# Kernel optimization log

Measured on AMD Instinct MI355X. Metric: run time of the kernel, lower is better.

Reference implementation:

```python
import jax, jax.numpy as jnp
import numpy as np

B, N, D, S, H = 64, 4096, 256, 8, 512
ITERS = 3
EPS = 1e-8
SCALE = D ** -0.5
LN_EPS = 1e-5


def _ln(x, w, b):
    mu = jnp.mean(x, axis=-1, keepdims=True)
    var = jnp.var(x, axis=-1, keepdims=True)
    return (x - mu) * jax.lax.rsqrt(var + LN_EPS) * w + b


def setup_inputs() -> dict:
    key = jax.random.key(0)
    ks = jax.random.split(key, 20)
    g = lambda k, shape, s=0.02: jax.random.normal(k, shape, dtype=jnp.float32) * s
    return {
        "inputs": jax.random.normal(ks[0], (B, N, D), dtype=jnp.float32),
        "query_pos": jax.random.uniform(ks[1], (1, S, D), dtype=jnp.float32),
        "wq": g(ks[2], (D, D)), "bq": jnp.zeros((D,), jnp.float32),
        "wk": g(ks[3], (D, D)), "bk": jnp.zeros((D,), jnp.float32),
        "wv": g(ks[4], (D, D)), "bv": jnp.zeros((D,), jnp.float32),
        "w_ih": g(ks[5], (3 * D, D)), "b_ih": jnp.zeros((3 * D,), jnp.float32),
        "w_hh": g(ks[6], (3 * D, D)), "b_hh": jnp.zeros((3 * D,), jnp.float32),
        "w1": g(ks[7], (H, D)), "b1": jnp.zeros((H,), jnp.float32),
        "w2": g(ks[8], (D, H)), "b2": jnp.zeros((D,), jnp.float32),
        "ln_in_w": jnp.ones((D,), jnp.float32), "ln_in_b": jnp.zeros((D,), jnp.float32),
        "ln_s_w": jnp.ones((D,), jnp.float32), "ln_s_b": jnp.zeros((D,), jnp.float32),
        "ln_ff_w": jnp.ones((D,), jnp.float32), "ln_ff_b": jnp.zeros((D,), jnp.float32),
    }


def _step(slots, k, v, wq, bq, w_ih, b_ih, w_hh, b_hh, w1, b1, w2, b2,
          ln_s_w, ln_s_b, ln_ff_w, ln_ff_b):
    s = _ln(slots, ln_s_w, ln_s_b)
    q = s @ wq.T + bq                                  # [B,S,D]
    dots = jnp.einsum('bid,bjd->bij', q, k) * SCALE    # [B,S,N]
    attn = jax.nn.softmax(dots, axis=1) + EPS          # softmax over slots
    attn = attn / jnp.sum(attn, axis=-1, keepdims=True)
    updates = jnp.einsum('bjd,bij->bid', v, attn)      # [B,S,D]
    # GRUCell(input=updates, hidden=slots), PyTorch gate order r,z,n
    gx = updates @ w_ih.T + b_ih
    gh = slots @ w_hh.T + b_hh
    xr, xz, xn = jnp.split(gx, 3, axis=-1)
    hr, hz, hn = jnp.split(gh, 3, axis=-1)
    r = jax.nn.sigmoid(xr + hr)
    z = jax.nn.sigmoid(xz + hz)
    n = jnp.tanh(xn + r * hn)
    h = (1.0 - z) * n + z * slots
    ff = jnp.maximum(_ln(h, ln_ff_w, ln_ff_b) @ w1.T + b1, 0.0) @ w2.T + b2
    return h + ff


def reference(inputs, query_pos, wq, bq, wk, bk, wv, bv,
              w_ih, b_ih, w_hh, b_hh, w1, b1, w2, b2,
              ln_in_w, ln_in_b, ln_s_w, ln_s_b, ln_ff_w, ln_ff_b):
    b = inputs.shape[0]
    slots = jnp.broadcast_to(query_pos, (b, S, D))
    x = _ln(inputs, ln_in_w, ln_in_b)
    k = x @ wk.T + bk
    v = x @ wv.T + bv
    step = lambda s: _step(s, k, v, wq, bq, w_ih, b_ih, w_hh, b_hh,
                           w1, b1, w2, b2, ln_s_w, ln_s_b, ln_ff_w, ln_ff_b)
    for _ in range(ITERS):
        slots = step(slots)
    slots = step(jax.lax.stop_gradient(slots))
    return slots
```

## Files before the change

### kernel.cpp

```cpp
#include <hip/hip_runtime.h>
#include <hip/hip_bf16.h>

#define DEV __device__ __forceinline__
typedef unsigned short u16;
using s16x8  = __attribute__((ext_vector_type(8))) short;
using f32x4v = __attribute__((ext_vector_type(4))) float;

constexpr float SCALE  = 0.0625f;
constexpr float EPS    = 1e-8f;
constexpr float LN_EPS = 1e-5f;

DEV u16 f2bf(float f) {
    __hip_bfloat16 h = __float2bfloat16(f);
    u16 u; __builtin_memcpy(&u, &h, 2); return u;
}
DEV float bf2f(u16 u) {
    unsigned int x = ((unsigned int)u) << 16;
    float f; __builtin_memcpy(&f, &x, 4); return f;
}
DEV float ld1(const void* p, size_t i, int bf) {
    return bf ? bf2f(((const u16*)p)[i]) : ((const float*)p)[i];
}
DEV s16x8 pack8(float4 a, float4 b) {
    s16x8 o;
    o[0]=(short)f2bf(a.x); o[1]=(short)f2bf(a.y); o[2]=(short)f2bf(a.z); o[3]=(short)f2bf(a.w);
    o[4]=(short)f2bf(b.x); o[5]=(short)f2bf(b.y); o[6]=(short)f2bf(b.z); o[7]=(short)f2bf(b.w);
    return o;
}
DEV float warp_sum64(float v) {
    v += __shfl_xor(v, 1);  v += __shfl_xor(v, 2);  v += __shfl_xor(v, 4);
    v += __shfl_xor(v, 8);  v += __shfl_xor(v, 16); v += __shfl_xor(v, 32);
    return v;
}
DEV float sigf(float x) { return 1.f / (1.f + expf(-x)); }

__global__ void k_sniff(const void* __restrict__ x, int* __restrict__ flag) {
    int lane = threadIdx.x;
    u16 u = ((const u16*)x)[lane * 2];
    float v = bf2f(u);
    bool bad = !(fabsf(v) <= 1024.0f);
    unsigned long long m = __ballot(bad);
    if (lane == 0) *flag = (m == 0ull) ? 1 : 0;
}

__global__ __launch_bounds__(256) void k_prep_misc(
    const void* bq, const void* bk, const void* bv, const void* bih, const void* bhh,
    const void* b1, const void* b2, const void* liw, const void* lib,
    const void* lsw, const void* lsb, const void* lfw, const void* lfb,
    float* o_bq, float* o_bk, float* o_bv, float* o_bih, float* o_bhh,
    float* o_b1, float* o_b2, float* o_liw, float* o_lib,
    float* o_lsw, float* o_lsb, float* o_lfw, float* o_lfb,
    const int* flagp) {
    int bf = *flagp;
    int i = blockIdx.x * 256 + threadIdx.x;
    if (i < 256) { o_bq[i]  = ld1(bq,  i, bf); return; } i -= 256;
    if (i < 256) { o_bk[i]  = ld1(bk,  i, bf); return; } i -= 256;
    if (i < 256) { o_bv[i]  = ld1(bv,  i, bf); return; } i -= 256;
    if (i < 768) { o_bih[i] = ld1(bih, i, bf); return; } i -= 768;
    if (i < 768) { o_bhh[i] = ld1(bhh, i, bf); return; } i -= 768;
    if (i < 512) { o_b1[i]  = ld1(b1,  i, bf); return; } i -= 512;
    if (i < 256) { o_b2[i]  = ld1(b2,  i, bf); return; } i -= 256;
    if (i < 256) { o_liw[i] = ld1(liw, i, bf); return; } i -= 256;
    if (i < 256) { o_lib[i] = ld1(lib, i, bf); return; } i -= 256;
    if (i < 256) { o_lsw[i] = ld1(lsw, i, bf); return; } i -= 256;
    if (i < 256) { o_lsb[i] = ld1(lsb, i, bf); return; } i -= 256;
    if (i < 256) { o_lfw[i] = ld1(lfw, i, bf); return; } i -= 256;
    if (i < 256) { o_lfb[i] = ld1(lfb, i, bf); }
}

__global__ __launch_bounds__(256) void k_prep_w(
    const void* wq, const void* wv, const void* wk,
    const void* wih, const void* whh, const void* w1, const void* w2,
    u16* wqT_b, u16* wvT_b, u16* wk2_b, u16* wih_b, u16* whh_b, u16* w1_b, u16* w2_b,
    const float* __restrict__ liw, const int* flagp) {
    int bf = *flagp;
    int i = blockIdx.x * 256 + threadIdx.x;
    if (i < 65536)  { int c=i>>8, d=i&255; wqT_b[i] = f2bf(ld1(wq, (size_t)d*256+c, bf)); return; } i -= 65536;
    if (i < 65536)  { int c=i>>8, d=i&255; wvT_b[i] = f2bf(ld1(wv, (size_t)d*256+c, bf)); return; } i -= 65536;
    if (i < 65536)  { int n=i>>8, d=i&255; wk2_b[i] = f2bf(ld1(wk, (size_t)d*256+n, bf) * liw[n]); return; } i -= 65536;
    if (i < 196608) { wih_b[i] = f2bf(ld1(wih, i, bf)); return; } i -= 196608;
    if (i < 196608) { whh_b[i] = f2bf(ld1(whh, i, bf)); return; } i -= 196608;
    if (i < 131072) { w1_b[i]  = f2bf(ld1(w1,  i, bf)); return; } i -= 131072;
    if (i < 131072) { w2_b[i]  = f2bf(ld1(w2,  i, bf)); }
}

__global__ __launch_bounds__(256) void k_prep_m(const void* __restrict__ wk,
    const float* __restrict__ liw, const float* __restrict__ lib,
    const float* __restrict__ bk_f, float* __restrict__ m1p, float* __restrict__ m2p,
    const int* flagp) {
    int bf = *flagp;
    int wave = threadIdx.x >> 6, lane = threadIdx.x & 63;
    int d = blockIdx.x * 4 + wave;
    float s1 = 0.f, s2 = 0.f;
#pragma unroll
    for (int t = 0; t < 4; t++) {
        int c = lane * 4 + t;
        float w = ld1(wk, (size_t)d * 256 + c, bf);
        s1 += w * lib[c];
        s2 += w * liw[c];
    }
    s1 = warp_sum64(s1); s2 = warp_sum64(s2);
    if (lane == 0) { m1p[d] = s1 + bk_f[d]; m2p[d] = -s2; }
}

__global__ __launch_bounds__(256) void k_prep_u(
    const void* __restrict__ wq, const void* __restrict__ wk, const void* __restrict__ wih,
    const float* __restrict__ m1p, const float* __restrict__ m2p,
    const float* __restrict__ bq_f, const float* __restrict__ bv_f,
    const float* __restrict__ liw,
    float* __restrict__ u1, float* __restrict__ u2, float* __restrict__ bq2,
    float* __restrict__ wibv, float* __restrict__ c12, const int* flagp) {
    int bf = *flagp;
    int wave = threadIdx.x >> 6, lane = threadIdx.x & 63;
    int idx = blockIdx.x * 4 + wave;
    if (idx >= 1538) return;
    float s = 0.f;
#pragma unroll
    for (int t = 0; t < 4; t++) {
        int d = lane * 4 + t;
        if (idx < 256)       s += ld1(wq, (size_t)d*256 + idx, bf) * m1p[d];
        else if (idx < 512)  s += ld1(wq, (size_t)d*256 + (idx-256), bf) * m2p[d];
        else if (idx < 768)  s += bq_f[d] * ld1(wk, (size_t)d*256 + (idx-512), bf);
        else if (idx < 1536) s += ld1(wih, (size_t)(idx-768)*256 + d, bf) * bv_f[d];
        else if (idx == 1536) s += bq_f[d] * m1p[d];
        else                  s += bq_f[d] * m2p[d];
    }
    s = warp_sum64(s);
    if (lane == 0) {
        if (idx < 256)       u1[idx] = s;
        else if (idx < 512)  u2[idx-256] = s;
        else if (idx < 768)  bq2[idx-512] = s * liw[idx-512];
        else if (idx < 1536) wibv[idx-768] = s;
        else                 c12[idx-1536] = s;
    }
}

__global__ __launch_bounds__(256) void k_stats(const void* __restrict__ x,
                                               float* __restrict__ mu,
                                               float* __restrict__ rs,
                                               const int* flagp) {
    int bf = *flagp;
    int wave = threadIdx.x >> 6, lane = threadIdx.x & 63;
    int row  = blockIdx.x * 4 + wave;
    float v[4];
    if (bf) {
        u16 a4[4];
        __builtin_memcpy(a4, (const u16*)x + (size_t)row * 256 + lane * 4, 8);
#pragma unroll
        for (int i = 0; i < 4; i++) v[i] = bf2f(a4[i]);
    } else {
        float4 f = *(const float4*)((const float*)x + (size_t)row * 256 + lane * 4);
        v[0]=f.x; v[1]=f.y; v[2]=f.z; v[3]=f.w;
    }
    float s  = v[0]+v[1]+v[2]+v[3];
    float s2 = v[0]*v[0]+v[1]*v[1]+v[2]*v[2]+v[3]*v[3];
    s = warp_sum64(s); s2 = warp_sum64(s2);
    if (lane == 0) {
        float m = s * (1.f/256.f);
        mu[row] = m;
        rs[row] = rsqrtf(s2 * (1.f/256.f) - m*m + LN_EPS);
    }
}

__global__ __launch_bounds__(256) void k_prep_s(const void* __restrict__ qp,
    const float* __restrict__ lsw, const float* __restrict__ lsb,
    const float* __restrict__ u1, const float* __restrict__ u2, const float* __restrict__ c12,
    float* __restrict__ slots, u16* __restrict__ Acat, u16* __restrict__ s_b,
    float* __restrict__ kap, float* __restrict__ lam, const int* flagp) {
    int bf = *flagp;
    int m = blockIdx.x;
    int s_ = m & 7, d = threadIdx.x;
    float v = ld1(qp, (size_t)s_ * 256 + d, bf);
    slots[(size_t)m*256 + d]   = v;
    Acat[(size_t)m*512 + 256 + d] = f2bf(v);
    __shared__ float red[16];
    float su = warp_sum64(v), sq = warp_sum64(v*v);
    int wave = threadIdx.x >> 6, lane = threadIdx.x & 63;
    if (lane == 0) { red[wave] = su; red[4+wave] = sq; }
    __syncthreads();
    float S1 = red[0]+red[1]+red[2]+red[3], S2 = red[4]+red[5]+red[6]+red[7];
    float muv = S1*(1.f/256.f);
    float rsv = rsqrtf(S2*(1.f/256.f) - muv*muv + LN_EPS);
    float sn = (v - muv)*rsv*lsw[d] + lsb[d];
    s_b[(size_t)m*256 + d] = f2bf(sn);
    float ks = warp_sum64(sn * u1[d]), ls = warp_sum64(sn * u2[d]);
    if (lane == 0) { red[8+wave] = ks; red[12+wave] = ls; }
    __syncthreads();
    if (threadIdx.x == 0) {
        kap[m] = red[8]+red[9]+red[10]+red[11] + c12[0];
        lam[m] = red[12]+red[13]+red[14]+red[15] + c12[1];
    }
}

template<bool OUT_BF16, bool RELU>
__global__ __launch_bounds__(256) void gemm64(
    const u16* __restrict__ A, const u16* __restrict__ W,
    const float* __restrict__ bias, void* __restrict__ outp, int Nn, int K) {
    int m0 = blockIdx.x * 64, n0 = blockIdx.y * 64;
    int tid = threadIdx.x;
    int wave = tid >> 6, lane = tid & 63, quad = lane >> 4, l15 = lane & 15;
    int wm = wave >> 1, wn = wave & 1;
    __shared__ __attribute__((aligned(16))) u16 A_s[64*40];
    __shared__ __attribute__((aligned(16))) u16 B_s[64*40];
    f32x4v acc[2][2];
#pragma unroll
    for (int i = 0; i < 2; i++)
#pragma unroll
        for (int j = 0; j < 2; j++) acc[i][j] = (f32x4v){0.f,0.f,0.f,0.f};
    int r0 = tid >> 2, seg = tid & 3;
    int nkc = K >> 5;
    for (int kc = 0; kc < nkc; ++kc) {
        s16x8 a0 = *(const s16x8*)(A + (size_t)(m0 + r0)*K + kc*32 + seg*8);
        s16x8 b0 = *(const s16x8*)(W + (size_t)(n0 + r0)*K + kc*32 + seg*8);
        __syncthreads();
        *(s16x8*)(A_s + r0*40 + seg*8) = a0;
        *(s16x8*)(B_s + r0*40 + seg*8) = b0;
        __syncthreads();
        s16x8 af[2], bfr[2];
#pragma unroll
        for (int t = 0; t < 2; t++) af[t]  = *(const s16x8*)(A_s + (wm*32 + t*16 + l15)*40 + quad*8);
#pragma unroll
        for (int t = 0; t < 2; t++) bfr[t] = *(const s16x8*)(B_s + (wn*32 + t*16 + l15)*40 + quad*8);
#pragma unroll
        for (int ti = 0; ti < 2; ti++)
#pragma unroll
            for (int tj = 0; tj < 2; tj++)
                acc[ti][tj] = __builtin_amdgcn_mfma_f32_16x16x32_bf16(af[ti], bfr[tj], acc[ti][tj], 0, 0, 0);
    }
#pragma unroll
    for (int tj = 0; tj < 2; tj++) {
        int colg = n0 + wn*32 + tj*16 + l15;
        float bv_ = bias ? bias[colg] : 0.f;
#pragma unroll
        for (int ti = 0; ti < 2; ti++) {
            int rowb = m0 + wm*32 + ti*16 + quad*4;
#pragma unroll
            for (int r = 0; r < 4; r++) {
                float v = acc[ti][tj][r] + bv_;
                if (RELU) v = fmaxf(v, 0.f);
                if (OUT_BF16) ((u16*)outp)[(size_t)(rowb + r)*Nn + colg] = f2bf(v);
                else          ((float*)outp)[(size_t)(rowb + r)*Nn + colg] = v;
            }
        }
    }
}

__global__ __launch_bounds__(256) void k_big(const u16* __restrict__ Wc2_b,
    const u16* __restrict__ whh_b, const float* __restrict__ bih_f,
    const float* __restrict__ bhh_f, const float* __restrict__ wibv,
    u16* __restrict__ Wbig, float* __restrict__ bbig) {
    int idx = blockIdx.x * 256 + threadIdx.x;
    int n = idx >> 9, k = idx & 511;
    u16 v;
    if (n < 512)      v = (k < 256) ? Wc2_b[(size_t)n*256 + k] : whh_b[(size_t)n*256 + (k-256)];
    else if (n < 768) v = (k < 256) ? Wc2_b[(size_t)n*256 + k] : (u16)0;
    else              v = (k < 256) ? (u16)0 : whh_b[(size_t)(n-256)*256 + (k-256)];
    Wbig[idx] = v;
    if (idx < 1024) {
        float bb;
        if (idx < 512)      bb = bih_f[idx] + wibv[idx] + bhh_f[idx];
        else if (idx < 768) bb = bih_f[idx] + wibv[idx];
        else                bb = bhh_f[idx-256];
        bbig[idx] = bb;
    }
}

__global__ __launch_bounds__(256) void k_attn(
    const void* __restrict__ xraw, const u16* __restrict__ q2b,
    const float* __restrict__ kap, const float* __restrict__ lam,
    const float* __restrict__ mu, const float* __restrict__ rs,
    const int* __restrict__ flagp,
    float* __restrict__ Zp, float* __restrict__ Rp, float* __restrict__ Tp) {
    int bf = *flagp;
    int jcc = blockIdx.x;
    int b   = blockIdx.y;
    int tid = threadIdx.x;
    int wave = tid >> 6, lane = tid & 63, quad = lane >> 4, l15 = lane & 15;
    __shared__ __attribute__((aligned(16))) u16 q_s[16*264];
    __shared__ __attribute__((aligned(16))) u16 a_s[16*72];
    __shared__ __attribute__((aligned(16))) u16 T_s[32*520];
    __shared__ float kl_s[32];
    {
        int row = tid >> 5, seg = tid & 31;
        s16x8 qv = *(const s16x8*)(q2b + (size_t)(b*8 + row)*256 + seg*8);
        *(s16x8*)(q_s + row*264 + seg*8) = qv;
        s16x8 z = {0,0,0,0,0,0,0,0};
        *(s16x8*)(q_s + (8+row)*264 + seg*8) = z;
    }
    if (tid < 16) {
        kl_s[tid]      = (tid < 8) ? kap[b*8 + tid] : 0.f;
        kl_s[16 + tid] = (tid < 8) ? lam[b*8 + tid] : 0.f;
    }
    f32x4v accz[4];
#pragma unroll
    for (int t = 0; t < 4; t++) accz[t] = (f32x4v){0.f,0.f,0.f,0.f};
    float rtot[4] = {0.f,0.f,0.f,0.f}, ttot[4] = {0.f,0.f,0.f,0.f};

    for (int sub = 0; sub < 2; ++sub) {
        size_t jbase = (size_t)b*4096 + (size_t)(jcc*2 + sub)*64;
        __syncthreads();
#pragma unroll
        for (int it = 0; it < 8; ++it) {
            int j = it*8 + (tid >> 5);
            int cb = tid & 31;
            s16x8 val;
            if (bf) {
                val = *(const s16x8*)((const u16*)xraw + (jbase + j)*256 + cb*8);
            } else {
                const float4* sf = (const float4*)((const float*)xraw + (jbase + j)*256 + cb*8);
                float4 f0 = sf[0], f1 = sf[1];
                val = pack8(f0, f1);
            }
            *(s16x8*)(T_s + cb*520 + j*8) = val;
        }
        __syncthreads();
        f32x4v accd = (f32x4v){0.f,0.f,0.f,0.f};
        int jb16 = wave * 16;
#pragma unroll
        for (int kc = 0; kc < 8; ++kc) {
            s16x8 af = *(const s16x8*)(q_s + l15*264 + kc*32 + quad*8);
            s16x8 bv = *(const s16x8*)(T_s + (kc*4 + quad)*520 + (jb16 + l15)*8);
            accd = __builtin_amdgcn_mfma_f32_16x16x32_bf16(af, bv, accd, 0, 0, 0);
        }
        int jg = (int)jbase + jb16 + l15;
        float rsj = rs[jg], mrj = mu[jg] * rsj;
        float dv[4];
#pragma unroll
        for (int r = 0; r < 4; r++)
            dv[r] = SCALE*(rsj*accd[r] + mrj*kl_s[16 + quad*4 + r] + kl_s[quad*4 + r]);
        float mx = fmaxf(fmaxf(dv[0], dv[1]), fmaxf(dv[2], dv[3]));
        mx = fmaxf(mx, __shfl_xor(mx, 16));
        float ev[4];
        float sum = 0.f;
#pragma unroll
        for (int r = 0; r < 4; r++) { ev[r] = expf(dv[r] - mx); sum += ev[r]; }
        sum += __shfl_xor(sum, 16);
        float inv = 1.f / sum;
#pragma unroll
        for (int r = 0; r < 4; r++) {
            float a = ev[r]*inv + EPS;
            rtot[r] += a;
            ttot[r] += a * mrj;
            a_s[(quad*4 + r)*72 + jb16 + l15] = f2bf(a * rsj);
        }
        __syncthreads();
#pragma unroll
        for (int kc2 = 0; kc2 < 2; ++kc2) {
            s16x8 af2 = *(const s16x8*)(a_s + l15*72 + kc2*32 + quad*8);
#pragma unroll
            for (int ct = 0; ct < 4; ++ct) {
                int c = wave*64 + ct*16 + l15;
                int cb = c >> 3, e = c & 7;
                s16x8 bv;
#pragma unroll
                for (int t = 0; t < 8; t++)
                    bv[t] = (short)T_s[cb*520 + (kc2*32 + quad*8 + t)*8 + e];
                accz[ct] = __builtin_amdgcn_mfma_f32_16x16x32_bf16(af2, bv, accz[ct], 0, 0, 0);
            }
        }
    }
    if (quad < 2) {
#pragma unroll
        for (int ct = 0; ct < 4; ++ct) {
            int c = wave*64 + ct*16 + l15;
#pragma unroll
            for (int r = 0; r < 4; r++)
                Zp[((size_t)(b*32 + jcc)*8 + quad*4 + r)*256 + c] = accz[ct][r];
        }
    }
#pragma unroll
    for (int r = 0; r < 4; r++) {
        rtot[r] += __shfl_xor(rtot[r], 1);
        rtot[r] += __shfl_xor(rtot[r], 2);
        rtot[r] += __shfl_xor(rtot[r], 4);
        rtot[r] += __shfl_xor(rtot[r], 8);
        ttot[r] += __shfl_xor(ttot[r], 1);
        ttot[r] += __shfl_xor(ttot[r], 2);
        ttot[r] += __shfl_xor(ttot[r], 4);
        ttot[r] += __shfl_xor(ttot[r], 8);
    }
    if (l15 == 0 && quad < 2) {
        int base = ((b*32 + jcc)*4 + wave)*8 + quad*4;
#pragma unroll
        for (int r = 0; r < 4; r++) { Rp[base + r] = rtot[r]; Tp[base + r] = ttot[r]; }
    }
}

__global__ __launch_bounds__(256) void k_reduce(const float* __restrict__ Zp,
    const float* __restrict__ Rp, const float* __restrict__ Tp,
    const float* __restrict__ liw, const float* __restrict__ lib,
    u16* __restrict__ Acat) {
    int m = blockIdx.x;
    int b = m >> 3, i = m & 7, d = threadIdx.x;
    float z = 0.f;
#pragma unroll
    for (int c = 0; c < 32; c++) z += Zp[((size_t)(b*32 + c)*8 + i)*256 + d];
    float rv = 0.f, tv = 0.f;
    if (d < 128) {
        rv = Rp[(size_t)(b*128 + d)*8 + i];
        tv = Tp[(size_t)(b*128 + d)*8 + i];
    }
    __shared__ float redR[4], redT[4];
    rv = warp_sum64(rv); tv = warp_sum64(tv);
    int wave = d >> 6, lane = d & 63;
    if (lane == 0) { redR[wave] = rv; redT[wave] = tv; }
    __syncthreads();
    float R = redR[0]+redR[1]+redR[2]+redR[3];
    float T = redT[0]+redT[1]+redT[2]+redT[3];
    float ys = (liw[d]*(z - T) + lib[d]*R) / R;
    Acat[(size_t)m*512 + d] = f2bf(ys);
}

__global__ __launch_bounds__(256) void k_gates(const float* __restrict__ g,
    const float* __restrict__ slots, const float* __restrict__ lfw,
    const float* __restrict__ lfb, float* __restrict__ h, u16* __restrict__ hln_b) {
    int m = blockIdx.x, d = threadIdx.x;
    const float* gm = g + (size_t)m*1024;
    float r = sigf(gm[d]);
    float z = sigf(gm[256 + d]);
    float nn = tanhf(gm[512 + d] + r * gm[768 + d]);
    float hv = (1.f - z)*nn + z*slots[(size_t)m*256 + d];
    h[(size_t)m*256 + d] = hv;
    __shared__ float red[8];
    float su = warp_sum64(hv), sq = warp_sum64(hv*hv);
    int wave = threadIdx.x >> 6, lane = threadIdx.x & 63;
    if (lane == 0) { red[wave] = su; red[4+wave] = sq; }
    __syncthreads();
    float S1 = red[0]+red[1]+red[2]+red[3], S2 = red[4]+red[5]+red[6]+red[7];
    float muv = S1*(1.f/256.f);
    float rsv = rsqrtf(S2*(1.f/256.f) - muv*muv + LN_EPS);
    hln_b[(size_t)m*256 + d] = f2bf((hv - muv)*rsv*lfw[d] + lfb[d]);
}

__global__ __launch_bounds__(256) void k_residual(const float* __restrict__ h,
    const float* __restrict__ ff2, const float* __restrict__ lsw,
    const float* __restrict__ lsb, const float* __restrict__ u1,
    const float* __restrict__ u2, const float* __restrict__ c12,
    float* __restrict__ slots, u16* __restrict__ Acat, u16* __restrict__ s_b,
    float* __restrict__ kap, float* __restrict__ lam) {
    int m = blockIdx.x, d = threadIdx.x;
    float sv = h[(size_t)m*256 + d] + ff2[(size_t)m*256 + d];
    slots[(size_t)m*256 + d] = sv;
    Acat[(size_t)m*512 + 256 + d] = f2bf(sv);
    __shared__ float red[16];
    float su = warp_sum64(sv), sq = warp_sum64(sv*sv);
    int wave = threadIdx.x >> 6, lane = threadIdx.x & 63;
    if (lane == 0) { red[wave] = su; red[4+wave] = sq; }
    __syncthreads();
    float S1 = red[0]+red[1]+red[2]+red[3], S2 = red[4]+red[5]+red[6]+red[7];
    float muv = S1*(1.f/256.f);
    float rsv = rsqrtf(S2*(1.f/256.f) - muv*muv + LN_EPS);
    float sn = (sv - muv)*rsv*lsw[d] + lsb[d];
    s_b[(size_t)m*256 + d] = f2bf(sn);
    float ks = warp_sum64(sn * u1[d]), ls = warp_sum64(sn * u2[d]);
    if (lane == 0) { red[8+wave] = ks; red[12+wave] = ls; }
    __syncthreads();
    if (threadIdx.x == 0) {
        kap[m] = red[8]+red[9]+red[10]+red[11] + c12[0];
        lam[m] = red[12]+red[13]+red[14]+red[15] + c12[1];
    }
}

__global__ __launch_bounds__(256) void k_out(const float* __restrict__ slots,
                                             void* __restrict__ out, const int* flagp) {
    int bf = *flagp;
    int i = blockIdx.x * 256 + threadIdx.x;
    if (bf) ((u16*)out)[i] = f2bf(slots[i]);
    else    ((float*)out)[i] = slots[i];
}

extern "C" void kernel_launch(void* const* d_in, const int* in_sizes, int n_in,
                              void* d_out, int out_size, void* d_ws, size_t ws_size,
                              hipStream_t stream) {
    (void)in_sizes; (void)n_in; (void)out_size; (void)ws_size;
    const void* inputs    = d_in[0];
    const void* query_pos = d_in[1];
    const void* wq   = d_in[2];  const void* bq   = d_in[3];
    const void* wk   = d_in[4];  const void* bk   = d_in[5];
    const void* wv   = d_in[6];  const void* bv   = d_in[7];
    const void* w_ih = d_in[8];  const void* b_ih = d_in[9];
    const void* w_hh = d_in[10]; const void* b_hh = d_in[11];
    const void* w1   = d_in[12]; const void* b1   = d_in[13];
    const void* w2   = d_in[14]; const void* b2   = d_in[15];
    const void* ln_in_w = d_in[16]; const void* ln_in_b = d_in[17];
    const void* ln_s_w  = d_in[18]; const void* ln_s_b  = d_in[19];
    const void* ln_ff_w = d_in[20]; const void* ln_ff_b = d_in[21];

    char* w = (char*)d_ws;
    size_t off = 0;
    auto alloc = [&](size_t bytes) -> void* {
        void* p = w + off;
        off = (off + bytes + 255) & ~(size_t)255;
        return p;
    };
    float* Zp     = (float*)alloc(16777216);
    float* gates  = (float*)alloc(2097152);
    u16*   Wbig_b = (u16*)alloc(1048576);
    u16*   Wc2_b  = (u16*)alloc(393216);
    u16*   Wc_b   = (u16*)alloc(131072);
    u16*   wqT_b  = (u16*)alloc(131072);
    u16*   wvT_b  = (u16*)alloc(131072);
    u16*   wk2_b  = (u16*)alloc(131072);
    u16*   wih_b  = (u16*)alloc(393216);
    u16*   whh_b  = (u16*)alloc(393216);
    u16*   w1_b   = (u16*)alloc(262144);
    u16*   w2_b   = (u16*)alloc(262144);
    float* mu     = (float*)alloc(1048576);
    float* rs     = (float*)alloc(1048576);
    float* slots  = (float*)alloc(524288);
    u16*   s_b    = (u16*)alloc(262144);
    u16*   Acat   = (u16*)alloc(524288);
    u16*   q2_b   = (u16*)alloc(262144);
    float* h      = (float*)alloc(524288);
    u16*   hln_b  = (u16*)alloc(262144);
    u16*   ff1_b  = (u16*)alloc(524288);
    float* ff2    = (float*)alloc(524288);
    float* Rp     = (float*)alloc(262144);
    float* Tp     = (float*)alloc(262144);
    float* bq_f   = (float*)alloc(1024);
    float* bk_f   = (float*)alloc(1024);
    float* bv_f   = (float*)alloc(1024);
    float* bih_f  = (float*)alloc(3072);
    float* bhh_f  = (float*)alloc(3072);
    float* b1_f   = (float*)alloc(2048);
    float* b2_f   = (float*)alloc(1024);
    float* liw_f  = (float*)alloc(1024);
    float* lib_f  = (float*)alloc(1024);
    float* lsw_f  = (float*)alloc(1024);
    float* lsb_f  = (float*)alloc(1024);
    float* lfw_f  = (float*)alloc(1024);
    float* lfb_f  = (float*)alloc(1024);
    float* m1p    = (float*)alloc(1024);
    float* m2p    = (float*)alloc(1024);
    float* u1     = (float*)alloc(1024);
    float* u2     = (float*)alloc(1024);
    float* bq2    = (float*)alloc(1024);
    float* wibv   = (float*)alloc(3072);
    float* bbig   = (float*)alloc(4096);
    float* c12    = (float*)alloc(256);
    float* kap    = (float*)alloc(2048);
    float* lam    = (float*)alloc(2048);
    int*   flag   = (int*)alloc(256);

    k_sniff<<<1, 64, 0, stream>>>(inputs, flag);
    k_prep_misc<<<18, 256, 0, stream>>>(bq, bk, bv, b_ih, b_hh, b1, b2,
                                        ln_in_w, ln_in_b, ln_s_w, ln_s_b, ln_ff_w, ln_ff_b,
                                        bq_f, bk_f, bv_f, bih_f, bhh_f, b1_f, b2_f,
                                        liw_f, lib_f, lsw_f, lsb_f, lfw_f, lfb_f, flag);
    k_stats<<<65536, 256, 0, stream>>>(inputs, mu, rs, flag);
    k_prep_w<<<3328, 256, 0, stream>>>(wq, wv, wk, w_ih, w_hh, w1, w2,
                                       wqT_b, wvT_b, wk2_b, wih_b, whh_b, w1_b, w2_b,
                                       liw_f, flag);
    k_prep_m<<<64, 256, 0, stream>>>(wk, liw_f, lib_f, bk_f, m1p, m2p, flag);
    k_prep_u<<<385, 256, 0, stream>>>(wq, wk, w_ih, m1p, m2p, bq_f, bv_f, liw_f,
                                      u1, u2, bq2, wibv, c12, flag);
    k_prep_s<<<512, 256, 0, stream>>>(query_pos, lsw_f, lsb_f, u1, u2, c12,
                                      slots, Acat, s_b, kap, lam, flag);
    gemm64<true, false><<<dim3(4, 4), 256, 0, stream>>>(wk2_b, wqT_b, nullptr, Wc_b, 256, 256);
    gemm64<true, false><<<dim3(12, 4), 256, 0, stream>>>(wih_b, wvT_b, nullptr, Wc2_b, 256, 256);
    k_big<<<2048, 256, 0, stream>>>(Wc2_b, whh_b, bih_f, bhh_f, wibv, Wbig_b, bbig);

    for (int step = 0; step < 4; ++step) {
        gemm64<true, false><<<dim3(8, 4), 256, 0, stream>>>(s_b, Wc_b, bq2, q2_b, 256, 256);
        k_attn<<<dim3(32, 64), 256, 0, stream>>>(inputs, q2_b, kap, lam, mu, rs, flag, Zp, Rp, Tp);
        k_reduce<<<512, 256, 0, stream>>>(Zp, Rp, Tp, liw_f, lib_f, Acat);
        gemm64<false, false><<<dim3(8, 16), 256, 0, stream>>>(Acat, Wbig_b, bbig, gates, 1024, 512);
        k_gates<<<512, 256, 0, stream>>>(gates, slots, lfw_f, lfb_f, h, hln_b);
        gemm64<true, true ><<<dim3(8, 8), 256, 0, stream>>>(hln_b, w1_b, b1_f, ff1_b, 512, 256);
        gemm64<false, false><<<dim3(8, 4), 256, 0, stream>>>(ff1_b, w2_b, b2_f, ff2, 256, 512);
        k_residual<<<512, 256, 0, stream>>>(h, ff2, lsw_f, lsb_f, u1, u2, c12,
                                            slots, Acat, s_b, kap, lam);
    }
    k_out<<<512, 256, 0, stream>>>(slots, d_out, flag);
}
```

Baseline: 809.6 us.

## Precompute bf16 row-major and transposed input copies once, reuse across attention steps

A new conversion kernel reads the input once, computes layernorm statistics, and writes both a bf16 row-major copy and a bf16 channel-major transposed copy. The attention kernel then loads MFMA operands directly from these copies instead of converting fp32 to bf16 and transposing through shared memory every iteration, and it drops the per-element scalar LDS gathers. This removes repeated conversion and LDS transpose work across the four steps. In exchange it adds 256 MB of workspace writes up front and keeps per-step global reads roughly as large.

```diff
diff --git a/kernel.cpp b/kernel.cpp
--- a/kernel.cpp
+++ b/kernel.cpp
@@ -20,12 +20,6 @@
 }
 DEV float ld1(const void* p, size_t i, int bf) {
     return bf ? bf2f(((const u16*)p)[i]) : ((const float*)p)[i];
-}
-DEV s16x8 pack8(float4 a, float4 b) {
-    s16x8 o;
-    o[0]=(short)f2bf(a.x); o[1]=(short)f2bf(a.y); o[2]=(short)f2bf(a.z); o[3]=(short)f2bf(a.w);
-    o[4]=(short)f2bf(b.x); o[5]=(short)f2bf(b.y); o[6]=(short)f2bf(b.z); o[7]=(short)f2bf(b.w);
-    return o;
 }
 DEV float warp_sum64(float v) {
     v += __shfl_xor(v, 1);  v += __shfl_xor(v, 2);  v += __shfl_xor(v, 4);
@@ -135,31 +129,56 @@
     }
 }
 
-__global__ __launch_bounds__(256) void k_stats(const void* __restrict__ x,
-                                               float* __restrict__ mu,
-                                               float* __restrict__ rs,
-                                               const int* flagp) {
-    int bf = *flagp;
-    int wave = threadIdx.x >> 6, lane = threadIdx.x & 63;
-    int row  = blockIdx.x * 4 + wave;
-    float v[4];
-    if (bf) {
-        u16 a4[4];
-        __builtin_memcpy(a4, (const u16*)x + (size_t)row * 256 + lane * 4, 8);
-#pragma unroll
-        for (int i = 0; i < 4; i++) v[i] = bf2f(a4[i]);
-    } else {
-        float4 f = *(const float4*)((const float*)x + (size_t)row * 256 + lane * 4);
-        v[0]=f.x; v[1]=f.y; v[2]=f.z; v[3]=f.w;
-    }
-    float s  = v[0]+v[1]+v[2]+v[3];
-    float s2 = v[0]*v[0]+v[1]*v[1]+v[2]*v[2]+v[3]*v[3];
-    s = warp_sum64(s); s2 = warp_sum64(s2);
-    if (lane == 0) {
-        float m = s * (1.f/256.f);
-        mu[row] = m;
-        rs[row] = rsqrtf(s2 * (1.f/256.f) - m*m + LN_EPS);
-    }
+__global__ __launch_bounds__(256) void k_conv(const void* __restrict__ x,
+    u16* __restrict__ XB, u16* __restrict__ XT,
+    float* __restrict__ mu, float* __restrict__ rs, const int* flagp) {
+    int bf = *flagp;
+    int jt = blockIdx.x;
+    int b  = blockIdx.y;
+    int tid = threadIdx.x;
+    int j = tid >> 2, q = tid & 3;
+    size_t rowg = (size_t)b * 4096 + jt * 64 + j;
+    __shared__ u16 LT[256 * 72];
+    float s = 0.f, s2 = 0.f;
+#pragma unroll
+    for (int cc = 0; cc < 16; ++cc) {
+        int c0 = cc * 16 + q * 4;
+        float v[4];
+        if (bf) {
+            u16 a4[4];
+            __builtin_memcpy(a4, (const u16*)x + rowg * 256 + c0, 8);
+#pragma unroll
+            for (int e = 0; e < 4; e++) v[e] = bf2f(a4[e]);
+        } else {
+            float4 f = *(const float4*)((const float*)x + rowg * 256 + c0);
+            v[0] = f.x; v[1] = f.y; v[2] = f.z; v[3] = f.w;
+        }
+        u16 b4[4];
+#pragma unroll
+        for (int e = 0; e < 4; e++) {
+            s += v[e]; s2 += v[e] * v[e];
+            b4[e] = f2bf(v[e]);
+            LT[(c0 + e) * 72 + j] = b4[e];
+        }
+        __builtin_memcpy(XB + rowg * 256 + c0, b4, 8);
+    }
+    s  += __shfl_xor(s, 1);   s  += __shfl_xor(s, 2);
+    s2 += __shfl_xor(s2, 1);  s2 += __shfl_xor(s2, 2);
+    if (q == 0) {
+        float m = s * (1.f / 256.f);
+        mu[rowg] = m;
+        rs[rowg] = rsqrtf(s2 * (1.f / 256.f) - m * m + LN_EPS);
+    }
+    __syncthreads();
+    int c = tid;
+    s16x8 seg[8];
+#pragma unroll
+    for (int k = 0; k < 8; ++k)
+        seg[k] = *(const s16x8*)(LT + c * 72 + k * 8);
+    u16* dst = XT + ((size_t)b * 256 + c) * 4096 + jt * 64;
+#pragma unroll
+    for (int k = 0; k < 8; ++k)
+        *(s16x8*)(dst + k * 8) = seg[k];
 }
 
 __global__ __launch_bounds__(256) void k_prep_s(const void* __restrict__ qp,
@@ -266,19 +285,17 @@
 }
 
 __global__ __launch_bounds__(256) void k_attn(
-    const void* __restrict__ xraw, const u16* __restrict__ q2b,
+    const u16* __restrict__ XB, const u16* __restrict__ XT,
+    const u16* __restrict__ q2b,
     const float* __restrict__ kap, const float* __restrict__ lam,
     const float* __restrict__ mu, const float* __restrict__ rs,
-    const int* __restrict__ flagp,
     float* __restrict__ Zp, float* __restrict__ Rp, float* __restrict__ Tp) {
-    int bf = *flagp;
     int jcc = blockIdx.x;
     int b   = blockIdx.y;
     int tid = threadIdx.x;
     int wave = tid >> 6, lane = tid & 63, quad = lane >> 4, l15 = lane & 15;
     __shared__ __attribute__((aligned(16))) u16 q_s[16*264];
     __shared__ __attribute__((aligned(16))) u16 a_s[16*72];
-    __shared__ __attribute__((aligned(16))) u16 T_s[32*520];
     __shared__ float kl_s[32];
     {
         int row = tid >> 5, seg = tid & 31;
@@ -291,39 +308,29 @@
         kl_s[tid]      = (tid < 8) ? kap[b*8 + tid] : 0.f;
         kl_s[16 + tid] = (tid < 8) ? lam[b*8 + tid] : 0.f;
     }
+    __syncthreads();
+
     f32x4v accz[4];
 #pragma unroll
     for (int t = 0; t < 4; t++) accz[t] = (f32x4v){0.f,0.f,0.f,0.f};
     float rtot[4] = {0.f,0.f,0.f,0.f}, ttot[4] = {0.f,0.f,0.f,0.f};
+    int jb16 = wave * 16;
+    const u16* xtb = XT + (size_t)b * 256 * 4096;
 
     for (int sub = 0; sub < 2; ++sub) {
-        size_t jbase = (size_t)b*4096 + (size_t)(jcc*2 + sub)*64;
-        __syncthreads();
-#pragma unroll
-        for (int it = 0; it < 8; ++it) {
-            int j = it*8 + (tid >> 5);
-            int cb = tid & 31;
-            s16x8 val;
-            if (bf) {
-                val = *(const s16x8*)((const u16*)xraw + (jbase + j)*256 + cb*8);
-            } else {
-                const float4* sf = (const float4*)((const float*)xraw + (jbase + j)*256 + cb*8);
-                float4 f0 = sf[0], f1 = sf[1];
-                val = pack8(f0, f1);
-            }
-            *(s16x8*)(T_s + cb*520 + j*8) = val;
-        }
-        __syncthreads();
+        int jloc = (jcc*2 + sub) * 64;
+        size_t rowg = (size_t)b*4096 + jloc + jb16 + l15;
+        const u16* xbp = XB + rowg*256 + quad*8;
+        s16x8 xv[8];
+#pragma unroll
+        for (int kc = 0; kc < 8; ++kc) xv[kc] = *(const s16x8*)(xbp + kc*32);
         f32x4v accd = (f32x4v){0.f,0.f,0.f,0.f};
-        int jb16 = wave * 16;
 #pragma unroll
         for (int kc = 0; kc < 8; ++kc) {
             s16x8 af = *(const s16x8*)(q_s + l15*264 + kc*32 + quad*8);
-            s16x8 bv = *(const s16x8*)(T_s + (kc*4 + quad)*520 + (jb16 + l15)*8);
-            accd = __builtin_amdgcn_mfma_f32_16x16x32_bf16(af, bv, accd, 0, 0, 0);
-        }
-        int jg = (int)jbase + jb16 + l15;
-        float rsj = rs[jg], mrj = mu[jg] * rsj;
+            accd = __builtin_amdgcn_mfma_f32_16x16x32_bf16(af, xv[kc], accd, 0, 0, 0);
+        }
+        float rsj = rs[rowg], mrj = mu[rowg] * rsj;
         float dv[4];
 #pragma unroll
         for (int r = 0; r < 4; r++)
@@ -336,26 +343,33 @@
         for (int r = 0; r < 4; r++) { ev[r] = expf(dv[r] - mx); sum += ev[r]; }
         sum += __shfl_xor(sum, 16);
         float inv = 1.f / sum;
+        float av[4];
 #pragma unroll
         for (int r = 0; r < 4; r++) {
             float a = ev[r]*inv + EPS;
             rtot[r] += a;
             ttot[r] += a * mrj;
-            a_s[(quad*4 + r)*72 + jb16 + l15] = f2bf(a * rsj);
+            av[r] = a * rsj;
+        }
+        s16x8 zv[8];
+#pragma unroll
+        for (int ct = 0; ct < 4; ++ct) {
+            int c = wave*64 + ct*16 + l15;
+#pragma unroll
+            for (int kc2 = 0; kc2 < 2; ++kc2)
+                zv[ct*2 + kc2] = *(const s16x8*)(xtb + (size_t)c*4096 + jloc + kc2*32 + quad*8);
         }
         __syncthreads();
 #pragma unroll
-        for (int kc2 = 0; kc2 < 2; ++kc2) {
-            s16x8 af2 = *(const s16x8*)(a_s + l15*72 + kc2*32 + quad*8);
-#pragma unroll
-            for (int ct = 0; ct < 4; ++ct) {
-                int c = wave*64 + ct*16 + l15;
-                int cb = c >> 3, e = c & 7;
-                s16x8 bv;
-#pragma unroll
-                for (int t = 0; t < 8; t++)
-                    bv[t] = (short)T_s[cb*520 + (kc2*32 + quad*8 + t)*8 + e];
-                accz[ct] = __builtin_amdgcn_mfma_f32_16x16x32_bf16(af2, bv, accz[ct], 0, 0, 0);
+        for (int r = 0; r < 4; r++)
+            a_s[(quad*4 + r)*72 + jb16 + l15] = f2bf(av[r]);
+        __syncthreads();
+#pragma unroll
+        for (int ct = 0; ct < 4; ++ct) {
+#pragma unroll
+            for (int kc2 = 0; kc2 < 2; ++kc2) {
+                s16x8 af2 = *(const s16x8*)(a_s + l15*72 + kc2*32 + quad*8);
+                accz[ct] = __builtin_amdgcn_mfma_f32_16x16x32_bf16(af2, zv[ct*2 + kc2], accz[ct], 0, 0, 0);
             }
         }
     }
@@ -493,6 +507,8 @@
         off = (off + bytes + 255) & ~(size_t)255;
         return p;
     };
+    u16*   XB     = (u16*)alloc(134217728);
+    u16*   XT     = (u16*)alloc(134217728);
     float* Zp     = (float*)alloc(16777216);
     float* gates  = (float*)alloc(2097152);
     u16*   Wbig_b = (u16*)alloc(1048576);
@@ -547,7 +563,7 @@
                                         ln_in_w, ln_in_b, ln_s_w, ln_s_b, ln_ff_w, ln_ff_b,
                                         bq_f, bk_f, bv_f, bih_f, bhh_f, b1_f, b2_f,
                                         liw_f, lib_f, lsw_f, lsb_f, lfw_f, lfb_f, flag);
-    k_stats<<<65536, 256, 0, stream>>>(inputs, mu, rs, flag);
+    k_conv<<<dim3(64, 64), 256, 0, stream>>>(inputs, XB, XT, mu, rs, flag);
     k_prep_w<<<3328, 256, 0, stream>>>(wq, wv, wk, w_ih, w_hh, w1, w2,
                                        wqT_b, wvT_b, wk2_b, wih_b, whh_b, w1_b, w2_b,
                                        liw_f, flag);
@@ -562,7 +578,7 @@
 
     for (int step = 0; step < 4; ++step) {
         gemm64<true, false><<<dim3(8, 4), 256, 0, stream>>>(s_b, Wc_b, bq2, q2_b, 256, 256);
-        k_attn<<<dim3(32, 64), 256, 0, stream>>>(inputs, q2_b, kap, lam, mu, rs, flag, Zp, Rp, Tp);
+        k_attn<<<dim3(32, 64), 256, 0, stream>>>(XB, XT, q2_b, kap, lam, mu, rs, Zp, Rp, Tp);
         k_reduce<<<512, 256, 0, stream>>>(Zp, Rp, Tp, liw_f, lib_f, Acat);
         gemm64<false, false><<<dim3(8, 16), 256, 0, stream>>>(Acat, Wbig_b, bbig, gates, 1024, 512);
         k_gates<<<512, 256, 0, stream>>>(gates, slots, lfw_f, lfb_f, h, hln_b);
```

Measured after the change: 899.4 us. 1.11x slower.

## Cache bf16 copy of inputs once and read it in attention steps

Applied to the files above, without the earlier changes.

The stats pass now writes a bf16 copy of the fp32 inputs to a 128 MB workspace, so each of the four attention steps reads half the bytes and skips the per-step fp32-to-bf16 conversion. The attention kernel also loads the dot-product B operand straight from global memory into registers, issues global loads before the barrier, pads the shared tile layout to cut LDS bank conflicts, and shrinks the query tile by zero-filling the unused MFMA rows in registers. The cost is one extra 128 MB write up front plus a larger workspace.

```diff
diff --git a/kernel.cpp b/kernel.cpp
--- a/kernel.cpp
+++ b/kernel.cpp
@@ -21,18 +21,14 @@
 DEV float ld1(const void* p, size_t i, int bf) {
     return bf ? bf2f(((const u16*)p)[i]) : ((const float*)p)[i];
 }
-DEV s16x8 pack8(float4 a, float4 b) {
-    s16x8 o;
-    o[0]=(short)f2bf(a.x); o[1]=(short)f2bf(a.y); o[2]=(short)f2bf(a.z); o[3]=(short)f2bf(a.w);
-    o[4]=(short)f2bf(b.x); o[5]=(short)f2bf(b.y); o[6]=(short)f2bf(b.z); o[7]=(short)f2bf(b.w);
-    return o;
-}
 DEV float warp_sum64(float v) {
     v += __shfl_xor(v, 1);  v += __shfl_xor(v, 2);  v += __shfl_xor(v, 4);
     v += __shfl_xor(v, 8);  v += __shfl_xor(v, 16); v += __shfl_xor(v, 32);
     return v;
 }
 DEV float sigf(float x) { return 1.f / (1.f + expf(-x)); }
+
+DEV int ts_addr(int cb, int j) { return cb*632 + j*8 + ((j>>3)<<4); }
 
 __global__ void k_sniff(const void* __restrict__ x, int* __restrict__ flag) {
     int lane = threadIdx.x;
@@ -136,6 +132,7 @@
 }
 
 __global__ __launch_bounds__(256) void k_stats(const void* __restrict__ x,
+                                               u16* __restrict__ XB,
                                                float* __restrict__ mu,
                                                float* __restrict__ rs,
                                                const int* flagp) {
@@ -151,6 +148,10 @@
     } else {
         float4 f = *(const float4*)((const float*)x + (size_t)row * 256 + lane * 4);
         v[0]=f.x; v[1]=f.y; v[2]=f.z; v[3]=f.w;
+        u16 b4[4];
+#pragma unroll
+        for (int i = 0; i < 4; i++) b4[i] = f2bf(v[i]);
+        __builtin_memcpy(XB + (size_t)row * 256 + lane * 4, b4, 8);
     }
     float s  = v[0]+v[1]+v[2]+v[3];
     float s2 = v[0]*v[0]+v[1]*v[1]+v[2]*v[2]+v[3]*v[3];
@@ -266,26 +267,26 @@
 }
 
 __global__ __launch_bounds__(256) void k_attn(
-    const void* __restrict__ xraw, const u16* __restrict__ q2b,
+    const void* __restrict__ xraw, const u16* __restrict__ XB,
+    const u16* __restrict__ q2b,
     const float* __restrict__ kap, const float* __restrict__ lam,
     const float* __restrict__ mu, const float* __restrict__ rs,
     const int* __restrict__ flagp,
     float* __restrict__ Zp, float* __restrict__ Rp, float* __restrict__ Tp) {
     int bf = *flagp;
+    const u16* xb = bf ? (const u16*)xraw : XB;
     int jcc = blockIdx.x;
     int b   = blockIdx.y;
     int tid = threadIdx.x;
     int wave = tid >> 6, lane = tid & 63, quad = lane >> 4, l15 = lane & 15;
-    __shared__ __attribute__((aligned(16))) u16 q_s[16*264];
+    __shared__ __attribute__((aligned(16))) u16 q_s[8*264];
     __shared__ __attribute__((aligned(16))) u16 a_s[16*72];
-    __shared__ __attribute__((aligned(16))) u16 T_s[32*520];
+    __shared__ __attribute__((aligned(16))) u16 T_s[32*632];
     __shared__ float kl_s[32];
     {
         int row = tid >> 5, seg = tid & 31;
         s16x8 qv = *(const s16x8*)(q2b + (size_t)(b*8 + row)*256 + seg*8);
         *(s16x8*)(q_s + row*264 + seg*8) = qv;
-        s16x8 z = {0,0,0,0,0,0,0,0};
-        *(s16x8*)(q_s + (8+row)*264 + seg*8) = z;
     }
     if (tid < 16) {
         kl_s[tid]      = (tid < 8) ? kap[b*8 + tid] : 0.f;
@@ -295,35 +296,38 @@
 #pragma unroll
     for (int t = 0; t < 4; t++) accz[t] = (f32x4v){0.f,0.f,0.f,0.f};
     float rtot[4] = {0.f,0.f,0.f,0.f}, ttot[4] = {0.f,0.f,0.f,0.f};
+    int jb16 = wave * 16;
+    int jrow = tid >> 5, cseg = tid & 31;
 
     for (int sub = 0; sub < 2; ++sub) {
-        size_t jbase = (size_t)b*4096 + (size_t)(jcc*2 + sub)*64;
+        int jloc = (jcc*2 + sub) * 64;
+        size_t jbase = (size_t)b*4096 + jloc;
+        s16x8 sv[8];
+#pragma unroll
+        for (int it = 0; it < 8; ++it) {
+            int j = it*8 + jrow;
+            sv[it] = *(const s16x8*)(xb + (jbase + j)*256 + cseg*8);
+        }
+        size_t rowg = jbase + jb16 + l15;
+        const u16* xbp = xb + rowg*256 + quad*8;
+        s16x8 xv[8];
+#pragma unroll
+        for (int kc = 0; kc < 8; ++kc) xv[kc] = *(const s16x8*)(xbp + kc*32);
         __syncthreads();
 #pragma unroll
         for (int it = 0; it < 8; ++it) {
-            int j = it*8 + (tid >> 5);
-            int cb = tid & 31;
-            s16x8 val;
-            if (bf) {
-                val = *(const s16x8*)((const u16*)xraw + (jbase + j)*256 + cb*8);
-            } else {
-                const float4* sf = (const float4*)((const float*)xraw + (jbase + j)*256 + cb*8);
-                float4 f0 = sf[0], f1 = sf[1];
-                val = pack8(f0, f1);
-            }
-            *(s16x8*)(T_s + cb*520 + j*8) = val;
-        }
-        __syncthreads();
+            int j = it*8 + jrow;
+            *(s16x8*)(T_s + ts_addr(cseg, j)) = sv[it];
+        }
         f32x4v accd = (f32x4v){0.f,0.f,0.f,0.f};
-        int jb16 = wave * 16;
 #pragma unroll
         for (int kc = 0; kc < 8; ++kc) {
-            s16x8 af = *(const s16x8*)(q_s + l15*264 + kc*32 + quad*8);
-            s16x8 bv = *(const s16x8*)(T_s + (kc*4 + quad)*520 + (jb16 + l15)*8);
-            accd = __builtin_amdgcn_mfma_f32_16x16x32_bf16(af, bv, accd, 0, 0, 0);
-        }
-        int jg = (int)jbase + jb16 + l15;
-        float rsj = rs[jg], mrj = mu[jg] * rsj;
+            s16x8 af;
+            if (l15 < 8) af = *(const s16x8*)(q_s + l15*264 + kc*32 + quad*8);
+            else         af = (s16x8){0,0,0,0,0,0,0,0};
+            accd = __builtin_amdgcn_mfma_f32_16x16x32_bf16(af, xv[kc], accd, 0, 0, 0);
+        }
+        float rsj = rs[rowg], mrj = mu[rowg] * rsj;
         float dv[4];
 #pragma unroll
         for (int r = 0; r < 4; r++)
@@ -345,16 +349,18 @@
         }
         __syncthreads();
 #pragma unroll
-        for (int kc2 = 0; kc2 < 2; ++kc2) {
-            s16x8 af2 = *(const s16x8*)(a_s + l15*72 + kc2*32 + quad*8);
-#pragma unroll
-            for (int ct = 0; ct < 4; ++ct) {
-                int c = wave*64 + ct*16 + l15;
-                int cb = c >> 3, e = c & 7;
+        for (int ct = 0; ct < 4; ++ct) {
+            int c = wave*64 + ct*16 + l15;
+            int cb = c >> 3, e = c & 7;
+#pragma unroll
+            for (int kc2 = 0; kc2 < 2; ++kc2) {
+                s16x8 af2 = *(const s16x8*)(a_s + l15*72 + kc2*32 + quad*8);
                 s16x8 bv;
 #pragma unroll
-                for (int t = 0; t < 8; t++)
-                    bv[t] = (short)T_s[cb*520 + (kc2*32 + quad*8 + t)*8 + e];
+                for (int t = 0; t < 8; t++) {
+                    int jj = kc2*32 + quad*8 + t;
+                    bv[t] = (short)T_s[ts_addr(cb, jj) + e];
+                }
                 accz[ct] = __builtin_amdgcn_mfma_f32_16x16x32_bf16(af2, bv, accz[ct], 0, 0, 0);
             }
         }
@@ -493,6 +499,7 @@
         off = (off + bytes + 255) & ~(size_t)255;
         return p;
     };
+    u16*   XB     = (u16*)alloc(134217728);
     float* Zp     = (float*)alloc(16777216);
     float* gates  = (float*)alloc(2097152);
     u16*   Wbig_b = (u16*)alloc(1048576);
@@ -547,7 +554,7 @@
                                         ln_in_w, ln_in_b, ln_s_w, ln_s_b, ln_ff_w, ln_ff_b,
                                         bq_f, bk_f, bv_f, bih_f, bhh_f, b1_f, b2_f,
                                         liw_f, lib_f, lsw_f, lsb_f, lfw_f, lfb_f, flag);
-    k_stats<<<65536, 256, 0, stream>>>(inputs, mu, rs, flag);
+    k_stats<<<65536, 256, 0, stream>>>(inputs, XB, mu, rs, flag);
     k_prep_w<<<3328, 256, 0, stream>>>(wq, wv, wk, w_ih, w_hh, w1, w2,
                                        wqT_b, wvT_b, wk2_b, wih_b, whh_b, w1_b, w2_b,
                                        liw_f, flag);
@@ -562,7 +569,7 @@
 
     for (int step = 0; step < 4; ++step) {
         gemm64<true, false><<<dim3(8, 4), 256, 0, stream>>>(s_b, Wc_b, bq2, q2_b, 256, 256);
-        k_attn<<<dim3(32, 64), 256, 0, stream>>>(inputs, q2_b, kap, lam, mu, rs, flag, Zp, Rp, Tp);
+        k_attn<<<dim3(32, 64), 256, 0, stream>>>(inputs, XB, q2_b, kap, lam, mu, rs, flag, Zp, Rp, Tp);
         k_reduce<<<512, 256, 0, stream>>>(Zp, Rp, Tp, liw_f, lib_f, Acat);
         gemm64<false, false><<<dim3(8, 16), 256, 0, stream>>>(Acat, Wbig_b, bbig, gates, 1024, 512);
         k_gates<<<512, 256, 0, stream>>>(gates, slots, lfw_f, lfb_f, h, hln_b);
```

Result: faster. 726.1 us (-10.3%).
